# Kernel tuning notes

Measured on AMD Instinct MI355X. Metric: run time of the kernel, lower is better.

The kernel has to match this reference:

```python
import jax, jax.numpy as jnp
import numpy as np

B, T_ENC, H, L, OUT, S_DEC = 32, 512, 512, 2, 128, 128
KV = 2 * H  # bidirectional encoder output width


def setup_inputs() -> dict:
    key = jax.random.key(0)
    ks = jax.random.split(key, 17)
    s = 0.05  # keep recurrent dynamics stable
    return {
        "encoder_output": jax.random.normal(ks[0], (B, T_ENC, KV), jnp.float32),
        "h0": jax.random.normal(ks[1], (L, B, H), jnp.float32) * s,
        "c0": jax.random.normal(ks[2], (L, B, H), jnp.float32) * s,
        "Wk": jax.random.normal(ks[3], (KV, KV), jnp.float32) * s,
        "Wq": jax.random.normal(ks[4], (KV, H), jnp.float32) * s,
        "Wv": jax.random.normal(ks[5], (KV, KV), jnp.float32) * s,
        "We": jax.random.normal(ks[6], (1, KV), jnp.float32) * s,
        "wih0": jax.random.normal(ks[7], (4 * H, OUT + KV), jnp.float32) * s,
        "whh0": jax.random.normal(ks[8], (4 * H, H), jnp.float32) * s,
        "bih0": jax.random.normal(ks[9], (4 * H,), jnp.float32) * s,
        "bhh0": jax.random.normal(ks[10], (4 * H,), jnp.float32) * s,
        "wih1": jax.random.normal(ks[11], (4 * H, H), jnp.float32) * s,
        "whh1": jax.random.normal(ks[12], (4 * H, H), jnp.float32) * s,
        "bih1": jax.random.normal(ks[13], (4 * H,), jnp.float32) * s,
        "bhh1": jax.random.normal(ks[14], (4 * H,), jnp.float32) * s,
        "fc_w": jax.random.normal(ks[15], (OUT, H), jnp.float32) * s,
        "fc_b": jax.random.normal(ks[16], (OUT,), jnp.float32) * s,
        "seq_length": S_DEC,
    }


def _lstm_cell(x, h, c, wih, whh, bih, bhh):
    # torch gate order: i, f, g, o
    g = x @ wih.T + h @ whh.T + bih + bhh
    i, f, gg, o = jnp.split(g, 4, axis=-1)
    c_new = jax.nn.sigmoid(f) * c + jax.nn.sigmoid(i) * jnp.tanh(gg)
    h_new = jax.nn.sigmoid(o) * jnp.tanh(c_new)
    return h_new, c_new


def reference(encoder_output, h0, c0, Wk, Wq, Wv, We, wih0, whh0, bih0, bhh0,
              wih1, whh1, bih1, bhh1, fc_w, fc_b, seq_length):
    # precomputed projections (key_layer / value_layer, no bias)
    key = encoder_output @ Wk.T      # [B, T_enc, KV]
    value = encoder_output @ Wv.T    # [B, T_enc, KV]

    def step(carry, _):
        h, c, y = carry  # h,c: [L,B,H]; y: [B,OUT]
        # Bahdanau attention, query = layer-0 hidden state
        q = h[0] @ Wq.T                                         # [B, KV]
        scores = jnp.einsum('btk,k->bt', jnp.tanh(q[:, None, :] + key), We[0])
        alpha = jax.nn.softmax(scores, axis=-1)                 # [B, T_enc]
        context = jnp.einsum('bt,btd->bd', alpha, value)        # [B, KV]
        x = jnp.concatenate([y, context], axis=-1)              # [B, OUT+KV]
        h0n, c0n = _lstm_cell(x, h[0], c[0], wih0, whh0, bih0, bhh0)
        h1n, c1n = _lstm_cell(h0n, h[1], c[1], wih1, whh1, bih1, bhh1)
        y_hat = jax.nn.relu(h1n @ fc_w.T + fc_b)                # [B, OUT]
        new_carry = (jnp.stack([h0n, h1n]), jnp.stack([c0n, c1n]), 1.0 + y_hat)
        return new_carry, y_hat

    y_init = jnp.zeros((h0.shape[1], fc_b.shape[0]), jnp.float32)  # SOS = 0.0
    _, ys = jax.lax.scan(step, (h0, c0, y_init), None, length=seq_length)
    return jnp.transpose(ys, (1, 0, 2))  # [B, seq_length, OUT]
```

## Files before the change

kernel.cpp:

```cpp
#include <hip/hip_runtime.h>
#include <hip/hip_bf16.h>
#include <cstdint>

#define TE    512
#define SD    128

typedef unsigned short u16;
typedef u16 u16x8 __attribute__((ext_vector_type(8)));

#define QO    0
#define SCO   32768
#define EBO   49152
#define CTXO  81920
#define YO    114688
#define H0O   118784
#define C0O   151552
#define H1O   184320
#define C1O   217088
#define ST_N  249856

__device__ __forceinline__ float b2f(u16 v) { return __uint_as_float(((unsigned)v) << 16); }
__device__ __forceinline__ u16 f2b(float f) {
  unsigned u = __float_as_uint(f);
  return (u16)((u + 0x7FFFu + ((u >> 16) & 1u)) >> 16);
}
__device__ __forceinline__ float tanh_f(float x) {
  float xc = fminf(12.f, fmaxf(-12.f, x));
  float e  = __expf(2.f * xc);
  return __fdividef(e - 1.f, e + 1.f);
}
__device__ __forceinline__ float sigm(float x) {
  float xc = fminf(30.f, fmaxf(-30.f, x));
  return __fdividef(1.f, 1.f + __expf(-xc));
}

template<bool KF32>
__global__ __launch_bounds__(256)
void gemm_k(const float* __restrict__ E, const float* __restrict__ Wk, void* __restrict__ keyp) {
  __shared__ float Asm[16][68], Bsm[16][68];
  const int tid = threadIdx.x;
  const int tm = blockIdx.x * 64, tn = blockIdx.y * 64;
  const int lr = tid >> 2, lc = (tid & 3) * 4;
  const int tx = tid & 15, ty = tid >> 4;
  float acc[4][4] = {};
  for (int k0 = 0; k0 < 1024; k0 += 16) {
    float4 av = *(const float4*)(&E[(long)(tm + lr) * 1024 + k0 + lc]);
    float4 bv = *(const float4*)(&Wk[(long)(tn + lr) * 1024 + k0 + lc]);
    Asm[lc][lr] = av.x; Asm[lc + 1][lr] = av.y; Asm[lc + 2][lr] = av.z; Asm[lc + 3][lr] = av.w;
    Bsm[lc][lr] = bv.x; Bsm[lc + 1][lr] = bv.y; Bsm[lc + 2][lr] = bv.z; Bsm[lc + 3][lr] = bv.w;
    __syncthreads();
#pragma unroll
    for (int kk = 0; kk < 16; ++kk) {
      float4 a4 = *(const float4*)(&Asm[kk][ty * 4]);
      float4 b4 = *(const float4*)(&Bsm[kk][tx * 4]);
      acc[0][0] += a4.x * b4.x; acc[0][1] += a4.x * b4.y; acc[0][2] += a4.x * b4.z; acc[0][3] += a4.x * b4.w;
      acc[1][0] += a4.y * b4.x; acc[1][1] += a4.y * b4.y; acc[1][2] += a4.y * b4.z; acc[1][3] += a4.y * b4.w;
      acc[2][0] += a4.z * b4.x; acc[2][1] += a4.z * b4.y; acc[2][2] += a4.z * b4.z; acc[2][3] += a4.z * b4.w;
      acc[3][0] += a4.w * b4.x; acc[3][1] += a4.w * b4.y; acc[3][2] += a4.w * b4.z; acc[3][3] += a4.w * b4.w;
    }
    __syncthreads();
  }
#pragma unroll
  for (int i = 0; i < 4; ++i)
#pragma unroll
    for (int j = 0; j < 4; ++j) {
      long idx = (long)(tm + ty * 4 + i) * 1024 + tn + tx * 4 + j;
      if constexpr (KF32) ((float*)keyp)[idx] = acc[i][j];
      else                ((u16*)keyp)[idx]   = f2b(acc[i][j]);
    }
}

__global__ __launch_bounds__(256)
void init_state(const float* __restrict__ h0, const float* __restrict__ c0, float* __restrict__ st) {
  int i = blockIdx.x * 256 + threadIdx.x;
  st[H0O + i] = h0[i];
  st[H1O + i] = h0[16384 + i];
  st[C0O + i] = c0[i];
  st[C1O + i] = c0[16384 + i];
  if (i < 4096) st[YO + i] = 0.f;
}

__global__ __launch_bounds__(256)
void qproj(const float* __restrict__ h0, const float* __restrict__ Wq, float* __restrict__ st) {
  __shared__ float hr[512];
  const int b = blockIdx.x >> 2, o = (blockIdx.x & 3) * 256 + threadIdx.x;
  for (int i = threadIdx.x; i < 512; i += 256) hr[i] = h0[b * 512 + i];
  __syncthreads();
  float acc = 0.f;
  for (int k = 0; k < 512; k += 4) {
    float4 wv = *(const float4*)(&Wq[(long)o * 512 + k]);
    acc += hr[k] * wv.x + hr[k + 1] * wv.y + hr[k + 2] * wv.z + hr[k + 3] * wv.w;
  }
  st[QO + b * 1024 + o] = acc;
}

template<bool KF32>
__global__ __launch_bounds__(256)
void stepA(const void* __restrict__ keyp, const float* __restrict__ We, float* __restrict__ st) {
  const int tid = threadIdx.x, wv = tid >> 6, ln = tid & 63;
  const int b = blockIdx.x >> 4, tc = blockIdx.x & 15, t0 = tc * 32;
  float qr[16], wer[16];
  {
    const float* qp = st + QO + b * 1024 + ln * 16;
#pragma unroll
    for (int j = 0; j < 16; ++j) qr[j] = qp[j];
#pragma unroll
    for (int j = 0; j < 16; j += 4) {
      float4 w4 = *(const float4*)(&We[ln * 16 + j]);
      wer[j] = w4.x; wer[j + 1] = w4.y; wer[j + 2] = w4.z; wer[j + 3] = w4.w;
    }
  }
  for (int tt = wv; tt < 32; tt += 4) {
    const long kbase = ((long)(b * TE + t0 + tt) << 10) + ln * 16;
    float kv[16];
    if constexpr (KF32) {
      const float* kr = (const float*)keyp + kbase;
#pragma unroll
      for (int j = 0; j < 16; j += 4) {
        float4 k4 = *(const float4*)(kr + j);
        kv[j] = k4.x; kv[j + 1] = k4.y; kv[j + 2] = k4.z; kv[j + 3] = k4.w;
      }
    } else {
      const u16* kr = (const u16*)keyp + kbase;
      u16x8 k0 = *(const u16x8*)kr;
      u16x8 k1 = *(const u16x8*)(kr + 8);
#pragma unroll
      for (int j = 0; j < 8; ++j) { kv[j] = b2f(k0[j]); kv[8 + j] = b2f(k1[j]); }
    }
    float part = 0.f;
#pragma unroll
    for (int j = 0; j < 16; ++j) part += tanh_f(qr[j] + kv[j]) * wer[j];
    for (int off = 32; off; off >>= 1) part += __shfl_down(part, off);
    if (ln == 0) st[SCO + b * 512 + t0 + tt] = part;
  }
}

__global__ __launch_bounds__(256)
void stepB(const float* __restrict__ E, float* __restrict__ st) {
  __shared__ float al[512];
  __shared__ float rr[8];
  __shared__ float gp[8 * 132];
  const int tid = threadIdx.x, wv = tid >> 6, ln = tid & 63;
  const int b = blockIdx.x >> 3, dc = blockIdx.x & 7;
  al[tid]       = st[SCO + b * 512 + tid];
  al[tid + 256] = st[SCO + b * 512 + tid + 256];
  __syncthreads();
  float m = fmaxf(al[tid], al[tid + 256]);
  for (int off = 32; off; off >>= 1) m = fmaxf(m, __shfl_xor(m, off));
  if (ln == 0) rr[wv] = m;
  __syncthreads();
  const float M = fmaxf(fmaxf(rr[0], rr[1]), fmaxf(rr[2], rr[3]));
  float e0 = __expf(al[tid] - M), e1 = __expf(al[tid + 256] - M);
  float l = e0 + e1;
  for (int off = 32; off; off >>= 1) l += __shfl_xor(l, off);
  if (ln == 0) rr[4 + wv] = l;
  __syncthreads();
  const float inv = __fdividef(1.f, rr[4] + rr[5] + rr[6] + rr[7]);
  al[tid] = e0; al[tid + 256] = e1;
  __syncthreads();
  const int dl = (tid & 31) * 4;
  const int tg = tid >> 5;
  float a0 = 0.f, a1 = 0.f, a2 = 0.f, a3 = 0.f;
  const float* Eb = E + ((long)b * TE) * 1024 + dc * 128 + dl;
  for (int t = tg; t < 512; t += 8) {
    float4 ev = *(const float4*)(Eb + (long)t * 1024);
    float av = al[t];
    a0 += av * ev.x; a1 += av * ev.y; a2 += av * ev.z; a3 += av * ev.w;
  }
  float4 av4 = {a0, a1, a2, a3};
  *(float4*)(&gp[tg * 132 + dl]) = av4;
  __syncthreads();
  if (tid < 128) {
    float s = 0.f;
#pragma unroll
    for (int g = 0; g < 8; ++g) s += gp[g * 132 + tid];
    st[EBO + b * 1024 + dc * 128 + tid] = s * inv;
  }
}

__global__ __launch_bounds__(256)
void stepC(const float* __restrict__ Wv, const float* __restrict__ fcw,
           const float* __restrict__ fcb, float* __restrict__ st,
           float* __restrict__ out, int s) {
  const int tid = threadIdx.x, wv = tid >> 6, ln = tid & 63;
  if (blockIdx.x < 64) {
    __shared__ float ebs[32 * 132];
    __shared__ float wvs[16 * 132];
    const int och = blockIdx.x * 16;
    const int o = tid >> 4;
    const int b0 = (tid & 15) * 2;
    float acc0 = 0.f, acc1 = 0.f;
    for (int dch = 0; dch < 8; ++dch) {
#pragma unroll
      for (int i = 0; i < 4; ++i) {
        int idx = tid * 4 + i * 1024;
        int bb = idx >> 7, dd = idx & 127;
        *(float4*)(&ebs[bb * 132 + dd]) = *(const float4*)(st + EBO + bb * 1024 + dch * 128 + dd);
      }
      {
        int r = tid >> 4, c = (tid & 15) * 8;
        const float* wp = &Wv[(long)(och + r) * 1024 + dch * 128 + c];
        float4 wa = *(const float4*)wp;
        float4 wb = *(const float4*)(wp + 4);
        *(float4*)(&wvs[r * 132 + c])     = wa;
        *(float4*)(&wvs[r * 132 + c + 4]) = wb;
      }
      __syncthreads();
#pragma unroll
      for (int j = 0; j < 128; j += 4) {
        float4 w4 = *(const float4*)(&wvs[o * 132 + j]);
        float4 x0 = *(const float4*)(&ebs[b0 * 132 + j]);
        float4 x1 = *(const float4*)(&ebs[(b0 + 1) * 132 + j]);
        acc0 += x0.x * w4.x + x0.y * w4.y + x0.z * w4.z + x0.w * w4.w;
        acc1 += x1.x * w4.x + x1.y * w4.y + x1.z * w4.z + x1.w * w4.w;
      }
      __syncthreads();
    }
    st[CTXO + b0 * 1024 + och + o]       = acc0;
    st[CTXO + (b0 + 1) * 1024 + och + o] = acc1;
  } else if (s > 0) {
    __shared__ float h1s[512];
    const int b = blockIdx.x - 64;
    const int p = s & 1;
    for (int i = tid; i < 512; i += 256) h1s[i] = st[H1O + p * 16384 + b * 512 + i];
    __syncthreads();
#pragma unroll
    for (int oi = 0; oi < 32; ++oi) {
      const int o = wv * 32 + oi;
      float part = 0.f;
#pragma unroll
      for (int kk = 0; kk < 8; ++kk) {
        int k = kk * 64 + ln;
        part += h1s[k] * fcw[(long)o * 512 + k];
      }
      for (int off = 32; off; off >>= 1) part += __shfl_down(part, off);
      if (ln == 0) {
        float yh = fmaxf(part + fcb[o], 0.f);
        out[((long)b * SD + (s - 1)) * 128 + o] = yh;
        st[YO + b * 128 + o] = 1.f + yh;
      }
    }
  }
}

__global__ __launch_bounds__(256)
void stepD(const float* __restrict__ wih0, const float* __restrict__ whh0,
           const float* __restrict__ bih0, const float* __restrict__ bhh0,
           float* __restrict__ st, int p) {
  __shared__ float xs[32 * 132];
  __shared__ float wr[8 * 132];
  __shared__ float gp[4 * 32 * 8];
  const int tid = threadIdx.x, wv = tid >> 6, ln = tid & 63;
  const int h0d = blockIdx.x * 2;
  float acc[8];
#pragma unroll
  for (int r = 0; r < 8; ++r) acc[r] = 0.f;

  for (int ch = 0; ch < 13; ++ch) {
    const float* src; int stride, col0;
    if (ch == 0)      { src = st + YO;               stride = 128;  col0 = 0; }
    else if (ch <= 8) { src = st + CTXO;             stride = 1024; col0 = (ch - 1) * 128; }
    else              { src = st + H0O + p * 16384;  stride = 512;  col0 = (ch - 9) * 128; }
#pragma unroll
    for (int i = 0; i < 4; ++i) {
      int e4 = tid * 4 + i * 1024;
      int bs = e4 >> 7, j = e4 & 127;
      *(float4*)(&xs[bs * 132 + j]) = *(const float4*)(src + bs * stride + col0 + j);
    }
    {
      int e = tid * 4, r = e >> 7, j = e & 127;
      int g = r >> 1, hh = r & 1;
      const float* wsrc; long rb;
      if (ch <= 8) { wsrc = wih0; rb = (long)(g * 512 + h0d + hh) * 1152 + ch * 128; }
      else         { wsrc = whh0; rb = (long)(g * 512 + h0d + hh) * 512 + (ch - 9) * 128; }
      *(float4*)(&wr[r * 132 + j]) = *(const float4*)(&wsrc[rb + j]);
    }
    __syncthreads();
    const int b = tid & 31, j0 = (tid >> 5) * 16;
#pragma unroll
    for (int jj = 0; jj < 16; jj += 4) {
      const float4 xv = *(const float4*)(&xs[b * 132 + j0 + jj]);
#pragma unroll
      for (int r = 0; r < 8; ++r) {
        const float4 w4 = *(const float4*)(&wr[r * 132 + j0 + jj]);
        acc[r] += xv.x * w4.x + xv.y * w4.y + xv.z * w4.z + xv.w * w4.w;
      }
    }
    __syncthreads();
  }
#pragma unroll
  for (int r = 0; r < 8; ++r) acc[r] += __shfl_down(acc[r], 32);
  if (ln < 32) {
#pragma unroll
    for (int r = 0; r < 8; ++r) gp[(wv * 32 + ln) * 8 + r] = acc[r];
  }
  __syncthreads();
  if (tid < 64) {
    const int b = tid & 31, hh = tid >> 5, h = h0d + hh;
    float gg[4];
#pragma unroll
    for (int g = 0; g < 4; ++g) {
      int r = g * 2 + hh;
      gg[g] = gp[(0 * 32 + b) * 8 + r] + gp[(1 * 32 + b) * 8 + r] +
              gp[(2 * 32 + b) * 8 + r] + gp[(3 * 32 + b) * 8 + r] +
              bih0[g * 512 + h] + bhh0[g * 512 + h];
    }
    float ig = sigm(gg[0]), fg = sigm(gg[1]), gt = tanh_f(gg[2]), og = sigm(gg[3]);
    int si = b * 512 + h;
    float c  = st[C0O + p * 16384 + si];
    float cn = fg * c + ig * gt;
    float hn = og * tanh_f(cn);
    st[H0O + (p ^ 1) * 16384 + si] = hn;
    st[C0O + (p ^ 1) * 16384 + si] = cn;
  }
}

__global__ __launch_bounds__(256)
void stepE(const float* __restrict__ wih1, const float* __restrict__ whh1,
           const float* __restrict__ bih1, const float* __restrict__ bhh1,
           const float* __restrict__ Wq, float* __restrict__ st, int p) {
  __shared__ float xs[32 * 132];
  __shared__ float wr[12 * 132];
  __shared__ float gp[4 * 32 * 12];
  const int tid = threadIdx.x, wv = tid >> 6, ln = tid & 63;
  const int h0d = blockIdx.x * 2;
  float acc[12];
#pragma unroll
  for (int r = 0; r < 12; ++r) acc[r] = 0.f;

  for (int ch = 0; ch < 8; ++ch) {
    const float* src = (ch < 4) ? (st + H0O + (p ^ 1) * 16384) : (st + H1O + p * 16384);
    const int col0 = (ch & 3) * 128;
#pragma unroll
    for (int i = 0; i < 4; ++i) {
      int e4 = tid * 4 + i * 1024;
      int bs = e4 >> 7, j = e4 & 127;
      *(float4*)(&xs[bs * 132 + j]) = *(const float4*)(src + bs * 512 + col0 + j);
    }
    {
      int e = tid * 4, r = e >> 7, j = e & 127;
      int g = r >> 1, hh = r & 1;
      const float* wsrc = (ch < 4) ? wih1 : whh1;
      long rb = (long)(g * 512 + h0d + hh) * 512 + col0;
      *(float4*)(&wr[r * 132 + j]) = *(const float4*)(&wsrc[rb + j]);
      if (ch < 4 && tid < 128) {
        int rq = e >> 7, j2 = e & 127;
        long rqb = (long)(4 * blockIdx.x + rq) * 512 + col0;
        *(float4*)(&wr[(8 + rq) * 132 + j2]) = *(const float4*)(&Wq[rqb + j2]);
      }
    }
    __syncthreads();
    const int b = tid & 31, j0 = (tid >> 5) * 16;
#pragma unroll
    for (int jj = 0; jj < 16; jj += 4) {
      const float4 xv = *(const float4*)(&xs[b * 132 + j0 + jj]);
#pragma unroll
      for (int r = 0; r < 8; ++r) {
        const float4 w4 = *(const float4*)(&wr[r * 132 + j0 + jj]);
        acc[r] += xv.x * w4.x + xv.y * w4.y + xv.z * w4.z + xv.w * w4.w;
      }
      if (ch < 4) {
#pragma unroll
        for (int r = 8; r < 12; ++r) {
          const float4 w4 = *(const float4*)(&wr[r * 132 + j0 + jj]);
          acc[r] += xv.x * w4.x + xv.y * w4.y + xv.z * w4.z + xv.w * w4.w;
        }
      }
    }
    __syncthreads();
  }
#pragma unroll
  for (int r = 0; r < 12; ++r) acc[r] += __shfl_down(acc[r], 32);
  if (ln < 32) {
#pragma unroll
    for (int r = 0; r < 12; ++r) gp[(wv * 32 + ln) * 12 + r] = acc[r];
  }
  __syncthreads();
  if (tid < 64) {
    const int b = tid & 31, hh = tid >> 5, h = h0d + hh;
    float gg[4];
#pragma unroll
    for (int g = 0; g < 4; ++g) {
      int r = g * 2 + hh;
      gg[g] = gp[(0 * 32 + b) * 12 + r] + gp[(1 * 32 + b) * 12 + r] +
              gp[(2 * 32 + b) * 12 + r] + gp[(3 * 32 + b) * 12 + r] +
              bih1[g * 512 + h] + bhh1[g * 512 + h];
    }
    float ig = sigm(gg[0]), fg = sigm(gg[1]), gt = tanh_f(gg[2]), og = sigm(gg[3]);
    int si = b * 512 + h;
    float c  = st[C1O + p * 16384 + si];
    float cn = fg * c + ig * gt;
    float hn = og * tanh_f(cn);
    st[H1O + (p ^ 1) * 16384 + si] = hn;
    st[C1O + (p ^ 1) * 16384 + si] = cn;
    int r0 = 8 + 2 * hh;
    float q0 = gp[(0 * 32 + b) * 12 + r0]     + gp[(1 * 32 + b) * 12 + r0] +
               gp[(2 * 32 + b) * 12 + r0]     + gp[(3 * 32 + b) * 12 + r0];
    float q1 = gp[(0 * 32 + b) * 12 + r0 + 1] + gp[(1 * 32 + b) * 12 + r0 + 1] +
               gp[(2 * 32 + b) * 12 + r0 + 1] + gp[(3 * 32 + b) * 12 + r0 + 1];
    int o0 = 4 * blockIdx.x + 2 * hh;
    st[QO + b * 1024 + o0]     = q0;
    st[QO + b * 1024 + o0 + 1] = q1;
  }
}

__global__ __launch_bounds__(256)
void fcK(const float* __restrict__ fcw, const float* __restrict__ fcb,
         float* __restrict__ st, float* __restrict__ out) {
  __shared__ float h1s[512];
  const int b = blockIdx.x >> 2, og = (blockIdx.x & 3) * 32;
  const int tid = threadIdx.x, wv = tid >> 6, ln = tid & 63;
  for (int i = tid; i < 512; i += 256) h1s[i] = st[H1O + b * 512 + i];
  __syncthreads();
#pragma unroll
  for (int oi = 0; oi < 8; ++oi) {
    const int o = og + wv * 8 + oi;
    float part = 0.f;
#pragma unroll
    for (int kk = 0; kk < 8; ++kk) {
      int k = kk * 64 + ln;
      part += h1s[k] * fcw[(long)o * 512 + k];
    }
    for (int off = 32; off; off >>= 1) part += __shfl_down(part, off);
    if (ln == 0) {
      float yh = fmaxf(part + fcb[o], 0.f);
      out[((long)b * SD + (SD - 1)) * 128 + o] = yh;
    }
  }
}

extern "C" void kernel_launch(void* const* d_in, const int* in_sizes, int n_in,
                              void* d_out, int out_size, void* d_ws, size_t ws_size,
                              hipStream_t stream) {
  (void)in_sizes; (void)n_in; (void)out_size;
  float* out = (float*)d_out;

  const float* E    = (const float*)d_in[0];
  const float* h0   = (const float*)d_in[1];
  const float* c0   = (const float*)d_in[2];
  const float* Wk   = (const float*)d_in[3];
  const float* Wq   = (const float*)d_in[4];
  const float* Wv   = (const float*)d_in[5];
  const float* We   = (const float*)d_in[6];
  const float* wih0 = (const float*)d_in[7];
  const float* whh0 = (const float*)d_in[8];
  const float* bih0 = (const float*)d_in[9];
  const float* bhh0 = (const float*)d_in[10];
  const float* wih1 = (const float*)d_in[11];
  const float* whh1 = (const float*)d_in[12];
  const float* bih1 = (const float*)d_in[13];
  const float* bhh1 = (const float*)d_in[14];
  const float* fcw  = (const float*)d_in[15];
  const float* fcb  = (const float*)d_in[16];

  const bool kf32 = ws_size >= (size_t)(16777216ull * 4 + ST_N * 4 + 4096);
  void* keyp = d_ws;
  float* st = kf32 ? ((float*)d_ws + 16777216) : ((float*)d_ws + 8388608);

  if (kf32) gemm_k<true ><<<dim3(256, 16), 256, 0, stream>>>(E, Wk, keyp);
  else      gemm_k<false><<<dim3(256, 16), 256, 0, stream>>>(E, Wk, keyp);
  init_state<<<64, 256, 0, stream>>>(h0, c0, st);
  qproj<<<128, 256, 0, stream>>>(h0, Wq, st);

  for (int s = 0; s < SD; ++s) {
    int p = s & 1;
    if (kf32) stepA<true ><<<512, 256, 0, stream>>>(keyp, We, st);
    else      stepA<false><<<512, 256, 0, stream>>>(keyp, We, st);
    stepB<<<256, 256, 0, stream>>>(E, st);
    stepC<<<96, 256, 0, stream>>>(Wv, fcw, fcb, st, out, s);
    stepD<<<256, 256, 0, stream>>>(wih0, whh0, bih0, bhh0, st, p);
    stepE<<<256, 256, 0, stream>>>(wih1, whh1, bih1, bhh1, Wq, st, p);
  }
  fcK<<<128, 256, 0, stream>>>(fcw, fcb, st, out);
}
```

Before: 14.57 ms.

## Fuse decode loop into one persistent kernel with grid barriers and bf16 value projection

Replaces the 640 per-step kernel launches with a single persistent kernel of 512 blocks that runs all decode steps, separated by atomic grid-wide barriers. It also precomputes value = E·Wvᵀ once in bf16, so each step reads the projected value directly instead of running a per-step Wv GEMM. The LSTM layers are re-split so each block handles one hidden unit, and the final FC runs on spare blocks while context is being computed. The cost is that all blocks must be co-resident for the spin barriers to avoid deadlock, and the value path loses precision from bf16 storage.

Result: slower. 57.18 ms (+292.6%).

```diff
diff --git a/kernel.cpp b/kernel.cpp
--- a/kernel.cpp
+++ b/kernel.cpp
@@ -4,8 +4,10 @@
 
 #define TE    512
 #define SD    128
+#define NB    512
 
 typedef unsigned short u16;
+typedef u16 u16x4 __attribute__((ext_vector_type(4)));
 typedef u16 u16x8 __attribute__((ext_vector_type(8)));
 
 #define QO    0
@@ -34,9 +36,8 @@
   return __fdividef(1.f, 1.f + __expf(-xc));
 }
 
-template<bool KF32>
-__global__ __launch_bounds__(256)
-void gemm_k(const float* __restrict__ E, const float* __restrict__ Wk, void* __restrict__ keyp) {
+__global__ __launch_bounds__(256)
+void gemm_nt(const float* __restrict__ A, const float* __restrict__ B, u16* __restrict__ outp) {
   __shared__ float Asm[16][68], Bsm[16][68];
   const int tid = threadIdx.x;
   const int tm = blockIdx.x * 64, tn = blockIdx.y * 64;
@@ -44,8 +45,8 @@
   const int tx = tid & 15, ty = tid >> 4;
   float acc[4][4] = {};
   for (int k0 = 0; k0 < 1024; k0 += 16) {
-    float4 av = *(const float4*)(&E[(long)(tm + lr) * 1024 + k0 + lc]);
-    float4 bv = *(const float4*)(&Wk[(long)(tn + lr) * 1024 + k0 + lc]);
+    float4 av = *(const float4*)(&A[(long)(tm + lr) * 1024 + k0 + lc]);
+    float4 bv = *(const float4*)(&B[(long)(tn + lr) * 1024 + k0 + lc]);
     Asm[lc][lr] = av.x; Asm[lc + 1][lr] = av.y; Asm[lc + 2][lr] = av.z; Asm[lc + 3][lr] = av.w;
     Bsm[lc][lr] = bv.x; Bsm[lc + 1][lr] = bv.y; Bsm[lc + 2][lr] = bv.z; Bsm[lc + 3][lr] = bv.w;
     __syncthreads();
@@ -63,11 +64,8 @@
 #pragma unroll
   for (int i = 0; i < 4; ++i)
 #pragma unroll
-    for (int j = 0; j < 4; ++j) {
-      long idx = (long)(tm + ty * 4 + i) * 1024 + tn + tx * 4 + j;
-      if constexpr (KF32) ((float*)keyp)[idx] = acc[i][j];
-      else                ((u16*)keyp)[idx]   = f2b(acc[i][j]);
-    }
+    for (int j = 0; j < 4; ++j)
+      outp[(long)(tm + ty * 4 + i) * 1024 + tn + tx * 4 + j] = f2b(acc[i][j]);
 }
 
 __global__ __launch_bounds__(256)
@@ -78,6 +76,7 @@
   st[C0O + i] = c0[i];
   st[C1O + i] = c0[16384 + i];
   if (i < 4096) st[YO + i] = 0.f;
+  if (i < 1024) ((int*)(st + EBO))[i] = 0;
 }
 
 __global__ __launch_bounds__(256)
@@ -94,9 +93,271 @@
   st[QO + b * 1024 + o] = acc;
 }
 
-template<bool KF32>
-__global__ __launch_bounds__(256)
-void stepA(const void* __restrict__ keyp, const float* __restrict__ We, float* __restrict__ st) {
+__device__ __forceinline__ void gbar(int* bar, int idx) {
+  __syncthreads();
+  if (threadIdx.x == 0) {
+    __threadfence();
+    __hip_atomic_fetch_add(&bar[idx], 1, __ATOMIC_RELEASE, __HIP_MEMORY_SCOPE_AGENT);
+    while (__hip_atomic_load(&bar[idx], __ATOMIC_ACQUIRE, __HIP_MEMORY_SCOPE_AGENT) < NB)
+      __builtin_amdgcn_s_sleep(1);
+    __threadfence();
+  }
+  __syncthreads();
+}
+
+__device__ void fc_do(const float* __restrict__ fcw, const float* __restrict__ fcb,
+                      float* __restrict__ st, float* __restrict__ out,
+                      int b, int srow, int hp, int tid, int wv, int ln, float* sm) {
+  float* h1s = sm;
+  for (int i = tid; i < 512; i += 256) h1s[i] = st[H1O + hp * 16384 + b * 512 + i];
+  __syncthreads();
+  for (int oi = 0; oi < 32; ++oi) {
+    const int o = wv * 32 + oi;
+    float part = 0.f;
+#pragma unroll
+    for (int kk = 0; kk < 8; ++kk) {
+      int k = kk * 64 + ln;
+      part += h1s[k] * fcw[(long)o * 512 + k];
+    }
+    for (int off = 32; off; off >>= 1) part += __shfl_down(part, off);
+    if (ln == 0) {
+      float yh = fmaxf(part + fcb[o], 0.f);
+      out[((long)b * SD + srow) * 128 + o] = yh;
+      st[YO + b * 128 + o] = 1.f + yh;
+    }
+  }
+  __syncthreads();
+}
+
+__global__ __launch_bounds__(256, 2)
+void decode_all(const u16* __restrict__ key, const u16* __restrict__ value,
+                const float* __restrict__ We, const float* __restrict__ Wq,
+                const float* __restrict__ wih0, const float* __restrict__ whh0,
+                const float* __restrict__ bih0, const float* __restrict__ bhh0,
+                const float* __restrict__ wih1, const float* __restrict__ whh1,
+                const float* __restrict__ bih1, const float* __restrict__ bhh1,
+                const float* __restrict__ fcw, const float* __restrict__ fcb,
+                float* __restrict__ st, float* __restrict__ out) {
+  __shared__ float sm[5792];
+  int* bar = (int*)(st + EBO);
+  const int bid = blockIdx.x, tid = threadIdx.x;
+  const int wv = tid >> 6, ln = tid & 63;
+
+  for (int s = 0; s < SD; ++s) {
+    const int p = s & 1;
+
+    {
+      const int b = bid >> 4, tc = bid & 15, t0 = tc * 32;
+      float qr[16], wer[16];
+      const float* qp = st + QO + b * 1024 + ln * 16;
+#pragma unroll
+      for (int j = 0; j < 16; ++j) qr[j] = qp[j];
+#pragma unroll
+      for (int j = 0; j < 16; j += 4) {
+        float4 w4 = *(const float4*)(&We[ln * 16 + j]);
+        wer[j] = w4.x; wer[j + 1] = w4.y; wer[j + 2] = w4.z; wer[j + 3] = w4.w;
+      }
+      for (int tt = wv; tt < 32; tt += 4) {
+        const u16* kr = key + ((long)(b * TE + t0 + tt) << 10) + ln * 16;
+        u16x8 k0 = *(const u16x8*)kr, k1 = *(const u16x8*)(kr + 8);
+        float part = 0.f;
+#pragma unroll
+        for (int j = 0; j < 8; ++j) part += tanh_f(qr[j] + b2f(k0[j])) * wer[j];
+#pragma unroll
+        for (int j = 0; j < 8; ++j) part += tanh_f(qr[8 + j] + b2f(k1[j])) * wer[8 + j];
+        for (int off = 32; off; off >>= 1) part += __shfl_down(part, off);
+        if (ln == 0) st[SCO + b * 512 + t0 + tt] = part;
+      }
+    }
+    gbar(bar, s * 4 + 0);
+
+    if (bid < 256) {
+      const int b = bid >> 3, dc = bid & 7;
+      float* al = sm; float* rr = sm + 512; float* gp = sm + 520;
+      al[tid]       = st[SCO + b * 512 + tid];
+      al[tid + 256] = st[SCO + b * 512 + tid + 256];
+      __syncthreads();
+      float m = fmaxf(al[tid], al[tid + 256]);
+      for (int off = 32; off; off >>= 1) m = fmaxf(m, __shfl_xor(m, off));
+      if (ln == 0) rr[wv] = m;
+      __syncthreads();
+      const float M = fmaxf(fmaxf(rr[0], rr[1]), fmaxf(rr[2], rr[3]));
+      float e0 = __expf(al[tid] - M), e1 = __expf(al[tid + 256] - M);
+      float l = e0 + e1;
+      for (int off = 32; off; off >>= 1) l += __shfl_xor(l, off);
+      if (ln == 0) rr[4 + wv] = l;
+      __syncthreads();
+      const float inv = __fdividef(1.f, rr[4] + rr[5] + rr[6] + rr[7]);
+      al[tid] = e0; al[tid + 256] = e1;
+      __syncthreads();
+      const int dl = (tid & 31) * 4, tg = tid >> 5;
+      float a0 = 0.f, a1 = 0.f, a2 = 0.f, a3 = 0.f;
+      const u16* vb = value + ((long)(b * TE) << 10) + dc * 128 + dl;
+      for (int t = tg; t < 512; t += 8) {
+        u16x4 vvv = *(const u16x4*)(vb + ((long)t << 10));
+        float av = al[t];
+        a0 += av * b2f(vvv[0]); a1 += av * b2f(vvv[1]);
+        a2 += av * b2f(vvv[2]); a3 += av * b2f(vvv[3]);
+      }
+      float4 a4 = {a0, a1, a2, a3};
+      *(float4*)(&gp[tg * 132 + dl]) = a4;
+      __syncthreads();
+      if (tid < 128) {
+        float ssum = 0.f;
+#pragma unroll
+        for (int g = 0; g < 8; ++g) ssum += gp[g * 132 + tid];
+        st[CTXO + b * 1024 + dc * 128 + tid] = ssum * inv;
+      }
+    } else if (bid < 288) {
+      if (s > 0) fc_do(fcw, fcb, st, out, bid - 256, s - 1, p, tid, wv, ln, sm);
+    }
+    gbar(bar, s * 4 + 1);
+
+    {
+      const int h = bid;
+      float* xs = sm; float* wr = sm + 4224; float* gp = sm + 4752;
+      float acc[4] = {0.f, 0.f, 0.f, 0.f};
+      for (int ch = 0; ch < 13; ++ch) {
+        const float* src; int stride, col0;
+        if (ch == 0)      { src = st + YO;               stride = 128;  col0 = 0; }
+        else if (ch <= 8) { src = st + CTXO;             stride = 1024; col0 = (ch - 1) * 128; }
+        else              { src = st + H0O + p * 16384;  stride = 512;  col0 = (ch - 9) * 128; }
+#pragma unroll
+        for (int i = 0; i < 4; ++i) {
+          int e4 = tid * 4 + i * 1024;
+          int bs = e4 >> 7, j = e4 & 127;
+          *(float4*)(&xs[bs * 132 + j]) = *(const float4*)(src + bs * stride + col0 + j);
+        }
+        {
+          int e = tid * 2, r = e >> 7, j = e & 127;
+          const float* wsrc; long rb;
+          if (ch <= 8) { wsrc = wih0; rb = (long)(r * 512 + h) * 1152 + ch * 128; }
+          else         { wsrc = whh0; rb = (long)(r * 512 + h) * 512 + (ch - 9) * 128; }
+          *(float2*)(&wr[r * 132 + j]) = *(const float2*)(&wsrc[rb + j]);
+        }
+        __syncthreads();
+        const int b = tid & 31, j0 = (tid >> 5) * 16;
+#pragma unroll
+        for (int jj = 0; jj < 16; jj += 4) {
+          const float4 xv = *(const float4*)(&xs[b * 132 + j0 + jj]);
+#pragma unroll
+          for (int r = 0; r < 4; ++r) {
+            const float4 w4 = *(const float4*)(&wr[r * 132 + j0 + jj]);
+            acc[r] += xv.x * w4.x + xv.y * w4.y + xv.z * w4.z + xv.w * w4.w;
+          }
+        }
+        __syncthreads();
+      }
+#pragma unroll
+      for (int r = 0; r < 4; ++r) acc[r] += __shfl_down(acc[r], 32);
+      if (ln < 32) {
+#pragma unroll
+        for (int r = 0; r < 4; ++r) gp[(wv * 32 + ln) * 4 + r] = acc[r];
+      }
+      __syncthreads();
+      if (tid < 32) {
+        const int b = tid;
+        float gg[4];
+#pragma unroll
+        for (int g = 0; g < 4; ++g)
+          gg[g] = gp[(0 * 32 + b) * 4 + g] + gp[(1 * 32 + b) * 4 + g] +
+                  gp[(2 * 32 + b) * 4 + g] + gp[(3 * 32 + b) * 4 + g] +
+                  bih0[g * 512 + h] + bhh0[g * 512 + h];
+        float ig = sigm(gg[0]), fg = sigm(gg[1]), gt = tanh_f(gg[2]), og = sigm(gg[3]);
+        int si = b * 512 + h;
+        float c  = st[C0O + p * 16384 + si];
+        float cn = fg * c + ig * gt;
+        float hn = og * tanh_f(cn);
+        st[H0O + (p ^ 1) * 16384 + si] = hn;
+        st[C0O + (p ^ 1) * 16384 + si] = cn;
+      }
+      __syncthreads();
+    }
+    gbar(bar, s * 4 + 2);
+
+    {
+      const int h = bid;
+      float* xs = sm; float* wr = sm + 4224; float* gp = sm + 5016;
+      float acc[6] = {0.f, 0.f, 0.f, 0.f, 0.f, 0.f};
+      for (int ch = 0; ch < 8; ++ch) {
+        const float* src = (ch < 4) ? (st + H0O + (p ^ 1) * 16384) : (st + H1O + p * 16384);
+        const int col0 = (ch & 3) * 128;
+#pragma unroll
+        for (int i = 0; i < 4; ++i) {
+          int e4 = tid * 4 + i * 1024;
+          int bs = e4 >> 7, j = e4 & 127;
+          *(float4*)(&xs[bs * 132 + j]) = *(const float4*)(src + bs * 512 + col0 + j);
+        }
+        {
+          int e = tid * 2, r = e >> 7, j = e & 127;
+          const float* wsrc = (ch < 4) ? wih1 : whh1;
+          long rb = (long)(r * 512 + h) * 512 + col0;
+          *(float2*)(&wr[r * 132 + j]) = *(const float2*)(&wsrc[rb + j]);
+          if (ch < 4) {
+            int rq = tid >> 7, j2 = tid & 127;
+            wr[(4 + rq) * 132 + j2] = Wq[(long)(2 * h + rq) * 512 + col0 + j2];
+          }
+        }
+        __syncthreads();
+        const int b = tid & 31, j0 = (tid >> 5) * 16;
+#pragma unroll
+        for (int jj = 0; jj < 16; jj += 4) {
+          const float4 xv = *(const float4*)(&xs[b * 132 + j0 + jj]);
+#pragma unroll
+          for (int r = 0; r < 4; ++r) {
+            const float4 w4 = *(const float4*)(&wr[r * 132 + j0 + jj]);
+            acc[r] += xv.x * w4.x + xv.y * w4.y + xv.z * w4.z + xv.w * w4.w;
+          }
+          if (ch < 4) {
+#pragma unroll
+            for (int r = 4; r < 6; ++r) {
+              const float4 w4 = *(const float4*)(&wr[r * 132 + j0 + jj]);
+              acc[r] += xv.x * w4.x + xv.y * w4.y + xv.z * w4.z + xv.w * w4.w;
+            }
+          }
+        }
+        __syncthreads();
+      }
+#pragma unroll
+      for (int r = 0; r < 6; ++r) acc[r] += __shfl_down(acc[r], 32);
+      if (ln < 32) {
+#pragma unroll
+        for (int r = 0; r < 6; ++r) gp[(wv * 32 + ln) * 6 + r] = acc[r];
+      }
+      __syncthreads();
+      if (tid < 32) {
+        const int b = tid;
+        float gg[4];
+#pragma unroll
+        for (int g = 0; g < 4; ++g)
+          gg[g] = gp[(0 * 32 + b) * 6 + g] + gp[(1 * 32 + b) * 6 + g] +
+                  gp[(2 * 32 + b) * 6 + g] + gp[(3 * 32 + b) * 6 + g] +
+                  bih1[g * 512 + h] + bhh1[g * 512 + h];
+        float ig = sigm(gg[0]), fg = sigm(gg[1]), gt = tanh_f(gg[2]), og = sigm(gg[3]);
+        int si = b * 512 + h;
+        float c  = st[C1O + p * 16384 + si];
+        float cn = fg * c + ig * gt;
+        float hn = og * tanh_f(cn);
+        st[H1O + (p ^ 1) * 16384 + si] = hn;
+        st[C1O + (p ^ 1) * 16384 + si] = cn;
+        float q0 = gp[(0 * 32 + b) * 6 + 4] + gp[(1 * 32 + b) * 6 + 4] +
+                   gp[(2 * 32 + b) * 6 + 4] + gp[(3 * 32 + b) * 6 + 4];
+        float q1 = gp[(0 * 32 + b) * 6 + 5] + gp[(1 * 32 + b) * 6 + 5] +
+                   gp[(2 * 32 + b) * 6 + 5] + gp[(3 * 32 + b) * 6 + 5];
+        st[QO + b * 1024 + 2 * h]     = q0;
+        st[QO + b * 1024 + 2 * h + 1] = q1;
+      }
+      __syncthreads();
+    }
+    gbar(bar, s * 4 + 3);
+  }
+
+  if (bid >= 256 && bid < 288)
+    fc_do(fcw, fcb, st, out, bid - 256, SD - 1, 0, tid, wv, ln, sm);
+}
+
+__global__ __launch_bounds__(256)
+void stepA2(const u16* __restrict__ key, const float* __restrict__ We, float* __restrict__ st) {
   const int tid = threadIdx.x, wv = tid >> 6, ln = tid & 63;
   const int b = blockIdx.x >> 4, tc = blockIdx.x & 15, t0 = tc * 32;
   float qr[16], wer[16];
@@ -111,32 +372,20 @@
     }
   }
   for (int tt = wv; tt < 32; tt += 4) {
-    const long kbase = ((long)(b * TE + t0 + tt) << 10) + ln * 16;
-    float kv[16];
-    if constexpr (KF32) {
-      const float* kr = (const float*)keyp + kbase;
-#pragma unroll
-      for (int j = 0; j < 16; j += 4) {
-        float4 k4 = *(const float4*)(kr + j);
-        kv[j] = k4.x; kv[j + 1] = k4.y; kv[j + 2] = k4.z; kv[j + 3] = k4.w;
-      }
-    } else {
-      const u16* kr = (const u16*)keyp + kbase;
-      u16x8 k0 = *(const u16x8*)kr;
-      u16x8 k1 = *(const u16x8*)(kr + 8);
-#pragma unroll
-      for (int j = 0; j < 8; ++j) { kv[j] = b2f(k0[j]); kv[8 + j] = b2f(k1[j]); }
-    }
+    const u16* kr = key + ((long)(b * TE + t0 + tt) << 10) + ln * 16;
+    u16x8 k0 = *(const u16x8*)kr, k1 = *(const u16x8*)(kr + 8);
     float part = 0.f;
 #pragma unroll
-    for (int j = 0; j < 16; ++j) part += tanh_f(qr[j] + kv[j]) * wer[j];
+    for (int j = 0; j < 8; ++j) part += tanh_f(qr[j] + b2f(k0[j])) * wer[j];
+#pragma unroll
+    for (int j = 0; j < 8; ++j) part += tanh_f(qr[8 + j] + b2f(k1[j])) * wer[8 + j];
     for (int off = 32; off; off >>= 1) part += __shfl_down(part, off);
     if (ln == 0) st[SCO + b * 512 + t0 + tt] = part;
   }
 }
 
 __global__ __launch_bounds__(256)
-void stepB(const float* __restrict__ E, float* __restrict__ st) {
+void stepB2(const float* __restrict__ E, float* __restrict__ st) {
   __shared__ float al[512];
   __shared__ float rr[8];
   __shared__ float gp[8 * 132];
@@ -179,9 +428,9 @@
 }
 
 __global__ __launch_bounds__(256)
-void stepC(const float* __restrict__ Wv, const float* __restrict__ fcw,
-           const float* __restrict__ fcb, float* __restrict__ st,
-           float* __restrict__ out, int s) {
+void stepC2(const float* __restrict__ Wv, const float* __restrict__ fcw,
+            const float* __restrict__ fcb, float* __restrict__ st,
+            float* __restrict__ out, int s) {
   const int tid = threadIdx.x, wv = tid >> 6, ln = tid & 63;
   if (blockIdx.x < 64) {
     __shared__ float ebs[32 * 132];
@@ -200,10 +449,8 @@
       {
         int r = tid >> 4, c = (tid & 15) * 8;
         const float* wp = &Wv[(long)(och + r) * 1024 + dch * 128 + c];
-        float4 wa = *(const float4*)wp;
-        float4 wb = *(const float4*)(wp + 4);
-        *(float4*)(&wvs[r * 132 + c])     = wa;
-        *(float4*)(&wvs[r * 132 + c + 4]) = wb;
+        *(float4*)(&wvs[r * 132 + c])     = *(const float4*)wp;
+        *(float4*)(&wvs[r * 132 + c + 4]) = *(const float4*)(wp + 4);
       }
       __syncthreads();
 #pragma unroll
@@ -244,9 +491,9 @@
 }
 
 __global__ __launch_bounds__(256)
-void stepD(const float* __restrict__ wih0, const float* __restrict__ whh0,
-           const float* __restrict__ bih0, const float* __restrict__ bhh0,
-           float* __restrict__ st, int p) {
+void stepD2(const float* __restrict__ wih0, const float* __restrict__ whh0,
+            const float* __restrict__ bih0, const float* __restrict__ bhh0,
+            float* __restrict__ st, int p) {
   __shared__ float xs[32 * 132];
   __shared__ float wr[8 * 132];
   __shared__ float gp[4 * 32 * 8];
@@ -255,7 +502,6 @@
   float acc[8];
 #pragma unroll
   for (int r = 0; r < 8; ++r) acc[r] = 0.f;
-
   for (int ch = 0; ch < 13; ++ch) {
     const float* src; int stride, col0;
     if (ch == 0)      { src = st + YO;               stride = 128;  col0 = 0; }
@@ -316,9 +562,9 @@
 }
 
 __global__ __launch_bounds__(256)
-void stepE(const float* __restrict__ wih1, const float* __restrict__ whh1,
-           const float* __restrict__ bih1, const float* __restrict__ bhh1,
-           const float* __restrict__ Wq, float* __restrict__ st, int p) {
+void stepE2(const float* __restrict__ wih1, const float* __restrict__ whh1,
+            const float* __restrict__ bih1, const float* __restrict__ bhh1,
+            const float* __restrict__ Wq, float* __restrict__ st, int p) {
   __shared__ float xs[32 * 132];
   __shared__ float wr[12 * 132];
   __shared__ float gp[4 * 32 * 12];
@@ -327,7 +573,6 @@
   float acc[12];
 #pragma unroll
   for (int r = 0; r < 12; ++r) acc[r] = 0.f;
-
   for (int ch = 0; ch < 8; ++ch) {
     const float* src = (ch < 4) ? (st + H0O + (p ^ 1) * 16384) : (st + H1O + p * 16384);
     const int col0 = (ch & 3) * 128;
@@ -405,8 +650,8 @@
 }
 
 __global__ __launch_bounds__(256)
-void fcK(const float* __restrict__ fcw, const float* __restrict__ fcb,
-         float* __restrict__ st, float* __restrict__ out) {
+void fcK2(const float* __restrict__ fcw, const float* __restrict__ fcb,
+          float* __restrict__ st, float* __restrict__ out) {
   __shared__ float h1s[512];
   const int b = blockIdx.x >> 2, og = (blockIdx.x & 3) * 32;
   const int tid = threadIdx.x, wv = tid >> 6, ln = tid & 63;
@@ -453,23 +698,32 @@
   const float* fcw  = (const float*)d_in[15];
   const float* fcb  = (const float*)d_in[16];
 
-  const bool kf32 = ws_size >= (size_t)(16777216ull * 4 + ST_N * 4 + 4096);
-  void* keyp = d_ws;
-  float* st = kf32 ? ((float*)d_ws + 16777216) : ((float*)d_ws + 8388608);
-
-  if (kf32) gemm_k<true ><<<dim3(256, 16), 256, 0, stream>>>(E, Wk, keyp);
-  else      gemm_k<false><<<dim3(256, 16), 256, 0, stream>>>(E, Wk, keyp);
-  init_state<<<64, 256, 0, stream>>>(h0, c0, st);
-  qproj<<<128, 256, 0, stream>>>(h0, Wq, st);
-
-  for (int s = 0; s < SD; ++s) {
-    int p = s & 1;
-    if (kf32) stepA<true ><<<512, 256, 0, stream>>>(keyp, We, st);
-    else      stepA<false><<<512, 256, 0, stream>>>(keyp, We, st);
-    stepB<<<256, 256, 0, stream>>>(E, st);
-    stepC<<<96, 256, 0, stream>>>(Wv, fcw, fcb, st, out, s);
-    stepD<<<256, 256, 0, stream>>>(wih0, whh0, bih0, bhh0, st, p);
-    stepE<<<256, 256, 0, stream>>>(wih1, whh1, bih1, bhh1, Wq, st, p);
-  }
-  fcK<<<128, 256, 0, stream>>>(fcw, fcb, st, out);
-}
+  const bool tier1 = ws_size >= (size_t)(16777216ull * 4 + ST_N * 4 + 4096);
+
+  if (tier1) {
+    u16* key   = (u16*)d_ws;
+    u16* value = key + 16777216;
+    float* st  = (float*)d_ws + 16777216;
+    gemm_nt<<<dim3(256, 16), 256, 0, stream>>>(E, Wk, key);
+    gemm_nt<<<dim3(256, 16), 256, 0, stream>>>(E, Wv, value);
+    init_state<<<64, 256, 0, stream>>>(h0, c0, st);
+    qproj<<<128, 256, 0, stream>>>(h0, Wq, st);
+    decode_all<<<NB, 256, 0, stream>>>(key, value, We, Wq, wih0, whh0, bih0, bhh0,
+                                       wih1, whh1, bih1, bhh1, fcw, fcb, st, out);
+  } else {
+    u16* key  = (u16*)d_ws;
+    float* st = (float*)d_ws + 8388608;
+    gemm_nt<<<dim3(256, 16), 256, 0, stream>>>(E, Wk, key);
+    init_state<<<64, 256, 0, stream>>>(h0, c0, st);
+    qproj<<<128, 256, 0, stream>>>(h0, Wq, st);
+    for (int s = 0; s < SD; ++s) {
+      int p = s & 1;
+      stepA2<<<512, 256, 0, stream>>>(key, We, st);
+      stepB2<<<256, 256, 0, stream>>>(E, st);
+      stepC2<<<96, 256, 0, stream>>>(Wv, fcw, fcb, st, out, s);
+      stepD2<<<256, 256, 0, stream>>>(wih0, whh0, bih0, bhh0, st, p);
+      stepE2<<<256, 256, 0, stream>>>(wih1, whh1, bih1, bhh1, Wq, st, p);
+    }
+    fcK2<<<128, 256, 0, stream>>>(fcw, fcb, st, out);
+  }
+}
```

## Precompute value projection once and read bf16 key/value in attention steps

Applied to the files above, without the earlier changes.

The value projection (encoder_output @ Wv^T) is now computed once up front alongside the key projection in a single batched GEMM. Attention then reduces over the projected values directly, which removes the per-step context GEMM against Wv and one kernel launch per decoder step. Key and value are always stored in bf16, halving per-step memory traffic, at the cost of extra rounding error and a larger one-time GEMM. stepA also processes two rows per iteration to raise instruction-level parallelism.

Result: faster. 12.08 ms (-17.0%).

```diff
diff --git a/kernel.cpp b/kernel.cpp
--- a/kernel.cpp
+++ b/kernel.cpp
@@ -6,11 +6,11 @@
 #define SD    128
 
 typedef unsigned short u16;
+typedef u16 u16x4 __attribute__((ext_vector_type(4)));
 typedef u16 u16x8 __attribute__((ext_vector_type(8)));
 
 #define QO    0
 #define SCO   32768
-#define EBO   49152
 #define CTXO  81920
 #define YO    114688
 #define H0O   118784
@@ -34,9 +34,11 @@
   return __fdividef(1.f, 1.f + __expf(-xc));
 }
 
-template<bool KF32>
-__global__ __launch_bounds__(256)
-void gemm_k(const float* __restrict__ E, const float* __restrict__ Wk, void* __restrict__ keyp) {
+__global__ __launch_bounds__(256)
+void gemm_kv(const float* __restrict__ E, const float* __restrict__ Wk,
+             const float* __restrict__ Wv, u16* __restrict__ key, u16* __restrict__ value) {
+  const float* B = blockIdx.z ? Wv : Wk;
+  u16* outp = blockIdx.z ? value : key;
   __shared__ float Asm[16][68], Bsm[16][68];
   const int tid = threadIdx.x;
   const int tm = blockIdx.x * 64, tn = blockIdx.y * 64;
@@ -45,7 +47,7 @@
   float acc[4][4] = {};
   for (int k0 = 0; k0 < 1024; k0 += 16) {
     float4 av = *(const float4*)(&E[(long)(tm + lr) * 1024 + k0 + lc]);
-    float4 bv = *(const float4*)(&Wk[(long)(tn + lr) * 1024 + k0 + lc]);
+    float4 bv = *(const float4*)(&B[(long)(tn + lr) * 1024 + k0 + lc]);
     Asm[lc][lr] = av.x; Asm[lc + 1][lr] = av.y; Asm[lc + 2][lr] = av.z; Asm[lc + 3][lr] = av.w;
     Bsm[lc][lr] = bv.x; Bsm[lc + 1][lr] = bv.y; Bsm[lc + 2][lr] = bv.z; Bsm[lc + 3][lr] = bv.w;
     __syncthreads();
@@ -63,11 +65,8 @@
 #pragma unroll
   for (int i = 0; i < 4; ++i)
 #pragma unroll
-    for (int j = 0; j < 4; ++j) {
-      long idx = (long)(tm + ty * 4 + i) * 1024 + tn + tx * 4 + j;
-      if constexpr (KF32) ((float*)keyp)[idx] = acc[i][j];
-      else                ((u16*)keyp)[idx]   = f2b(acc[i][j]);
-    }
+    for (int j = 0; j < 4; ++j)
+      outp[(long)(tm + ty * 4 + i) * 1024 + tn + tx * 4 + j] = f2b(acc[i][j]);
 }
 
 __global__ __launch_bounds__(256)
@@ -94,9 +93,8 @@
   st[QO + b * 1024 + o] = acc;
 }
 
-template<bool KF32>
-__global__ __launch_bounds__(256)
-void stepA(const void* __restrict__ keyp, const float* __restrict__ We, float* __restrict__ st) {
+__global__ __launch_bounds__(256)
+void stepA(const u16* __restrict__ key, const float* __restrict__ We, float* __restrict__ st) {
   const int tid = threadIdx.x, wv = tid >> 6, ln = tid & 63;
   const int b = blockIdx.x >> 4, tc = blockIdx.x & 15, t0 = tc * 32;
   float qr[16], wer[16];
@@ -110,117 +108,83 @@
       wer[j] = w4.x; wer[j + 1] = w4.y; wer[j + 2] = w4.z; wer[j + 3] = w4.w;
     }
   }
-  for (int tt = wv; tt < 32; tt += 4) {
-    const long kbase = ((long)(b * TE + t0 + tt) << 10) + ln * 16;
-    float kv[16];
-    if constexpr (KF32) {
-      const float* kr = (const float*)keyp + kbase;
-#pragma unroll
-      for (int j = 0; j < 16; j += 4) {
-        float4 k4 = *(const float4*)(kr + j);
-        kv[j] = k4.x; kv[j + 1] = k4.y; kv[j + 2] = k4.z; kv[j + 3] = k4.w;
-      }
-    } else {
-      const u16* kr = (const u16*)keyp + kbase;
-      u16x8 k0 = *(const u16x8*)kr;
-      u16x8 k1 = *(const u16x8*)(kr + 8);
-#pragma unroll
-      for (int j = 0; j < 8; ++j) { kv[j] = b2f(k0[j]); kv[8 + j] = b2f(k1[j]); }
-    }
-    float part = 0.f;
-#pragma unroll
-    for (int j = 0; j < 16; ++j) part += tanh_f(qr[j] + kv[j]) * wer[j];
-    for (int off = 32; off; off >>= 1) part += __shfl_down(part, off);
-    if (ln == 0) st[SCO + b * 512 + t0 + tt] = part;
-  }
-}
-
-__global__ __launch_bounds__(256)
-void stepB(const float* __restrict__ E, float* __restrict__ st) {
-  __shared__ float al[512];
-  __shared__ float rr[8];
-  __shared__ float gp[8 * 132];
-  const int tid = threadIdx.x, wv = tid >> 6, ln = tid & 63;
-  const int b = blockIdx.x >> 3, dc = blockIdx.x & 7;
-  al[tid]       = st[SCO + b * 512 + tid];
-  al[tid + 256] = st[SCO + b * 512 + tid + 256];
-  __syncthreads();
-  float m = fmaxf(al[tid], al[tid + 256]);
-  for (int off = 32; off; off >>= 1) m = fmaxf(m, __shfl_xor(m, off));
-  if (ln == 0) rr[wv] = m;
-  __syncthreads();
-  const float M = fmaxf(fmaxf(rr[0], rr[1]), fmaxf(rr[2], rr[3]));
-  float e0 = __expf(al[tid] - M), e1 = __expf(al[tid + 256] - M);
-  float l = e0 + e1;
-  for (int off = 32; off; off >>= 1) l += __shfl_xor(l, off);
-  if (ln == 0) rr[4 + wv] = l;
-  __syncthreads();
-  const float inv = __fdividef(1.f, rr[4] + rr[5] + rr[6] + rr[7]);
-  al[tid] = e0; al[tid + 256] = e1;
-  __syncthreads();
-  const int dl = (tid & 31) * 4;
-  const int tg = tid >> 5;
-  float a0 = 0.f, a1 = 0.f, a2 = 0.f, a3 = 0.f;
-  const float* Eb = E + ((long)b * TE) * 1024 + dc * 128 + dl;
-  for (int t = tg; t < 512; t += 8) {
-    float4 ev = *(const float4*)(Eb + (long)t * 1024);
-    float av = al[t];
-    a0 += av * ev.x; a1 += av * ev.y; a2 += av * ev.z; a3 += av * ev.w;
-  }
-  float4 av4 = {a0, a1, a2, a3};
-  *(float4*)(&gp[tg * 132 + dl]) = av4;
-  __syncthreads();
-  if (tid < 128) {
-    float s = 0.f;
-#pragma unroll
-    for (int g = 0; g < 8; ++g) s += gp[g * 132 + tid];
-    st[EBO + b * 1024 + dc * 128 + tid] = s * inv;
-  }
-}
-
-__global__ __launch_bounds__(256)
-void stepC(const float* __restrict__ Wv, const float* __restrict__ fcw,
+  const u16* kbase = key + ((long)(b * TE + t0) << 10) + ln * 16;
+#pragma unroll
+  for (int u = 0; u < 4; ++u) {
+    const int tt0 = wv + u * 8, tt1 = wv + u * 8 + 4;
+    const u16* kr0 = kbase + ((long)tt0 << 10);
+    const u16* kr1 = kbase + ((long)tt1 << 10);
+    u16x8 a0 = *(const u16x8*)kr0, a1 = *(const u16x8*)(kr0 + 8);
+    u16x8 b0 = *(const u16x8*)kr1, b1 = *(const u16x8*)(kr1 + 8);
+    float p0 = 0.f, p1 = 0.f;
+#pragma unroll
+    for (int j = 0; j < 8; ++j) {
+      p0 += tanh_f(qr[j] + b2f(a0[j])) * wer[j];
+      p1 += tanh_f(qr[j] + b2f(b0[j])) * wer[j];
+    }
+#pragma unroll
+    for (int j = 0; j < 8; ++j) {
+      p0 += tanh_f(qr[8 + j] + b2f(a1[j])) * wer[8 + j];
+      p1 += tanh_f(qr[8 + j] + b2f(b1[j])) * wer[8 + j];
+    }
+    for (int off = 32; off; off >>= 1) {
+      p0 += __shfl_down(p0, off);
+      p1 += __shfl_down(p1, off);
+    }
+    if (ln == 0) {
+      st[SCO + b * 512 + t0 + tt0] = p0;
+      st[SCO + b * 512 + t0 + tt1] = p1;
+    }
+  }
+}
+
+__global__ __launch_bounds__(256)
+void stepB(const u16* __restrict__ value, const float* __restrict__ fcw,
            const float* __restrict__ fcb, float* __restrict__ st,
            float* __restrict__ out, int s) {
+  __shared__ float sm[1576];
   const int tid = threadIdx.x, wv = tid >> 6, ln = tid & 63;
-  if (blockIdx.x < 64) {
-    __shared__ float ebs[32 * 132];
-    __shared__ float wvs[16 * 132];
-    const int och = blockIdx.x * 16;
-    const int o = tid >> 4;
-    const int b0 = (tid & 15) * 2;
-    float acc0 = 0.f, acc1 = 0.f;
-    for (int dch = 0; dch < 8; ++dch) {
-#pragma unroll
-      for (int i = 0; i < 4; ++i) {
-        int idx = tid * 4 + i * 1024;
-        int bb = idx >> 7, dd = idx & 127;
-        *(float4*)(&ebs[bb * 132 + dd]) = *(const float4*)(st + EBO + bb * 1024 + dch * 128 + dd);
-      }
-      {
-        int r = tid >> 4, c = (tid & 15) * 8;
-        const float* wp = &Wv[(long)(och + r) * 1024 + dch * 128 + c];
-        float4 wa = *(const float4*)wp;
-        float4 wb = *(const float4*)(wp + 4);
-        *(float4*)(&wvs[r * 132 + c])     = wa;
-        *(float4*)(&wvs[r * 132 + c + 4]) = wb;
-      }
-      __syncthreads();
-#pragma unroll
-      for (int j = 0; j < 128; j += 4) {
-        float4 w4 = *(const float4*)(&wvs[o * 132 + j]);
-        float4 x0 = *(const float4*)(&ebs[b0 * 132 + j]);
-        float4 x1 = *(const float4*)(&ebs[(b0 + 1) * 132 + j]);
-        acc0 += x0.x * w4.x + x0.y * w4.y + x0.z * w4.z + x0.w * w4.w;
-        acc1 += x1.x * w4.x + x1.y * w4.y + x1.z * w4.z + x1.w * w4.w;
-      }
-      __syncthreads();
-    }
-    st[CTXO + b0 * 1024 + och + o]       = acc0;
-    st[CTXO + (b0 + 1) * 1024 + och + o] = acc1;
+  if (blockIdx.x < 256) {
+    const int b = blockIdx.x >> 3, dc = blockIdx.x & 7;
+    float* al = sm; float* rr = sm + 512; float* gp = sm + 520;
+    al[tid]       = st[SCO + b * 512 + tid];
+    al[tid + 256] = st[SCO + b * 512 + tid + 256];
+    __syncthreads();
+    float m = fmaxf(al[tid], al[tid + 256]);
+    for (int off = 32; off; off >>= 1) m = fmaxf(m, __shfl_xor(m, off));
+    if (ln == 0) rr[wv] = m;
+    __syncthreads();
+    const float M = fmaxf(fmaxf(rr[0], rr[1]), fmaxf(rr[2], rr[3]));
+    float e0 = __expf(al[tid] - M), e1 = __expf(al[tid + 256] - M);
+    float l = e0 + e1;
+    for (int off = 32; off; off >>= 1) l += __shfl_xor(l, off);
+    if (ln == 0) rr[4 + wv] = l;
+    __syncthreads();
+    const float inv = __fdividef(1.f, rr[4] + rr[5] + rr[6] + rr[7]);
+    al[tid] = e0; al[tid + 256] = e1;
+    __syncthreads();
+    const int dl = (tid & 31) * 4, tg = tid >> 5;
+    float a0 = 0.f, a1 = 0.f, a2 = 0.f, a3 = 0.f;
+    const u16* vb = value + ((long)(b * TE) << 10) + dc * 128 + dl;
+#pragma unroll 4
+    for (int t = tg; t < 512; t += 8) {
+      u16x4 vvv = *(const u16x4*)(vb + ((long)t << 10));
+      float av = al[t];
+      a0 += av * b2f(vvv[0]); a1 += av * b2f(vvv[1]);
+      a2 += av * b2f(vvv[2]); a3 += av * b2f(vvv[3]);
+    }
+    float4 a4 = {a0, a1, a2, a3};
+    *(float4*)(&gp[tg * 132 + dl]) = a4;
+    __syncthreads();
+    if (tid < 128) {
+      float ssum = 0.f;
+#pragma unroll
+      for (int g = 0; g < 8; ++g) ssum += gp[g * 132 + tid];
+      st[CTXO + b * 1024 + dc * 128 + tid] = ssum * inv;
+    }
   } else if (s > 0) {
-    __shared__ float h1s[512];
-    const int b = blockIdx.x - 64;
+    float* h1s = sm;
+    const int b = blockIdx.x - 256;
     const int p = s & 1;
     for (int i = tid; i < 512; i += 256) h1s[i] = st[H1O + p * 16384 + b * 512 + i];
     __syncthreads();
@@ -244,7 +208,7 @@
 }
 
 __global__ __launch_bounds__(256)
-void stepD(const float* __restrict__ wih0, const float* __restrict__ whh0,
+void stepC(const float* __restrict__ wih0, const float* __restrict__ whh0,
            const float* __restrict__ bih0, const float* __restrict__ bhh0,
            float* __restrict__ st, int p) {
   __shared__ float xs[32 * 132];
@@ -255,7 +219,6 @@
   float acc[8];
 #pragma unroll
   for (int r = 0; r < 8; ++r) acc[r] = 0.f;
-
   for (int ch = 0; ch < 13; ++ch) {
     const float* src; int stride, col0;
     if (ch == 0)      { src = st + YO;               stride = 128;  col0 = 0; }
@@ -316,7 +279,7 @@
 }
 
 __global__ __launch_bounds__(256)
-void stepE(const float* __restrict__ wih1, const float* __restrict__ whh1,
+void stepD(const float* __restrict__ wih1, const float* __restrict__ whh1,
            const float* __restrict__ bih1, const float* __restrict__ bhh1,
            const float* __restrict__ Wq, float* __restrict__ st, int p) {
   __shared__ float xs[32 * 132];
@@ -327,7 +290,6 @@
   float acc[12];
 #pragma unroll
   for (int r = 0; r < 12; ++r) acc[r] = 0.f;
-
   for (int ch = 0; ch < 8; ++ch) {
     const float* src = (ch < 4) ? (st + H0O + (p ^ 1) * 16384) : (st + H1O + p * 16384);
     const int col0 = (ch & 3) * 128;
@@ -432,7 +394,7 @@
 extern "C" void kernel_launch(void* const* d_in, const int* in_sizes, int n_in,
                               void* d_out, int out_size, void* d_ws, size_t ws_size,
                               hipStream_t stream) {
-  (void)in_sizes; (void)n_in; (void)out_size;
+  (void)in_sizes; (void)n_in; (void)out_size; (void)ws_size;
   float* out = (float*)d_out;
 
   const float* E    = (const float*)d_in[0];
@@ -453,23 +415,20 @@
   const float* fcw  = (const float*)d_in[15];
   const float* fcb  = (const float*)d_in[16];
 
-  const bool kf32 = ws_size >= (size_t)(16777216ull * 4 + ST_N * 4 + 4096);
-  void* keyp = d_ws;
-  float* st = kf32 ? ((float*)d_ws + 16777216) : ((float*)d_ws + 8388608);
-
-  if (kf32) gemm_k<true ><<<dim3(256, 16), 256, 0, stream>>>(E, Wk, keyp);
-  else      gemm_k<false><<<dim3(256, 16), 256, 0, stream>>>(E, Wk, keyp);
+  u16* key   = (u16*)d_ws;
+  u16* value = key + 16777216;
+  float* st  = (float*)d_ws + 16777216;
+
+  gemm_kv<<<dim3(256, 16, 2), 256, 0, stream>>>(E, Wk, Wv, key, value);
   init_state<<<64, 256, 0, stream>>>(h0, c0, st);
   qproj<<<128, 256, 0, stream>>>(h0, Wq, st);
 
   for (int s = 0; s < SD; ++s) {
     int p = s & 1;
-    if (kf32) stepA<true ><<<512, 256, 0, stream>>>(keyp, We, st);
-    else      stepA<false><<<512, 256, 0, stream>>>(keyp, We, st);
-    stepB<<<256, 256, 0, stream>>>(E, st);
-    stepC<<<96, 256, 0, stream>>>(Wv, fcw, fcb, st, out, s);
-    stepD<<<256, 256, 0, stream>>>(wih0, whh0, bih0, bhh0, st, p);
-    stepE<<<256, 256, 0, stream>>>(wih1, whh1, bih1, bhh1, Wq, st, p);
+    stepA<<<512, 256, 0, stream>>>(key, We, st);
+    stepB<<<288, 256, 0, stream>>>(value, fcw, fcb, st, out, s);
+    stepC<<<256, 256, 0, stream>>>(wih0, whh0, bih0, bhh0, st, p);
+    stepD<<<256, 256, 0, stream>>>(wih1, whh1, bih1, bhh1, Wq, st, p);
   }
   fcK<<<128, 256, 0, stream>>>(fcw, fcb, st, out);
 }
```
